# Kernel optimization log

Measured on AMD Instinct MI355X. Metric: run time of the kernel, lower is better.

The kernel has to match this reference:

```python
import jax, jax.numpy as jnp
import numpy as np

N_NODES = 100000
N_EDGES = 1600000


def spmm(edge_index, edge_vals, x, n_nodes):
    # adj @ x with adj in COO form: out[dst] += val * x[src]
    src = edge_index[0]
    dst = edge_index[1]
    gathered = x[src] * edge_vals[:, None]  # [E, F]
    return jax.ops.segment_sum(gathered, dst, num_segments=n_nodes)


def setup_inputs() -> dict:
    key = jax.random.key(0)
    ks = jax.random.split(key, 8)
    x = jax.random.normal(ks[0], (N_NODES, 512), dtype=jnp.float32)
    edge_index = jax.random.randint(ks[1], (2, N_EDGES), 0, N_NODES, dtype=jnp.int64)
    edge_vals = jax.random.uniform(ks[2], (N_EDGES,), dtype=jnp.float32)
    # xavier-uniform style weights, zero biases (as in initialize_weights)
    def xavier(k, fan_in, fan_out):
        lim = float(np.sqrt(6.0 / (fan_in + fan_out)))
        return jax.random.uniform(k, (fan_in, fan_out), minval=-lim, maxval=lim, dtype=jnp.float32)
    W1 = xavier(ks[3], 512, 128)
    b1 = jnp.zeros((128,), jnp.float32)
    W2 = xavier(ks[4], 128, 64)
    b2 = jnp.zeros((64,), jnp.float32)
    W3 = xavier(ks[5], 64, 16)
    b3 = jnp.zeros((16,), jnp.float32)
    return {"x": x, "edge_index": edge_index, "edge_vals": edge_vals,
            "W1": W1, "b1": b1, "W2": W2, "b2": b2, "W3": W3, "b3": b3}


def reference(x, edge_index, edge_vals, W1, b1, W2, b2, W3, b3):
    n = x.shape[0]
    h = jax.nn.relu(spmm(edge_index, edge_vals, x @ W1 + b1, n))
    h = jax.nn.relu(spmm(edge_index, edge_vals, h @ W2 + b2, n))
    logits = spmm(edge_index, edge_vals, h @ W3 + b3, n)
    logp = jax.nn.log_softmax(logits, axis=1)
    return jnp.argmax(logp, axis=1)
```

## Files before the change

### kernel.cpp

```cpp
#include <hip/hip_runtime.h>

typedef _Float16 half8 __attribute__((ext_vector_type(8)));
typedef float floatx4 __attribute__((ext_vector_type(4)));

#define BSHIFT 7
#define BMASK 127
#define EPB 8192
#define P2CAP 4096

__device__ __forceinline__ void g2lds16(const void* g, void* l) {
    __builtin_amdgcn_global_load_lds(
        (const __attribute__((address_space(1))) void*)(unsigned long long)g,
        (__attribute__((address_space(3))) void*)(unsigned int)(unsigned long long)l,
        16, 0, 0);
}

__global__ __launch_bounds__(256) void k1_prep_hist(const float* __restrict__ W1,
                                                    const float* __restrict__ W2,
                                                    _Float16* __restrict__ w1hi,
                                                    _Float16* __restrict__ w1lo,
                                                    _Float16* __restrict__ w2hi,
                                                    _Float16* __restrict__ w2lo,
                                                    const int* __restrict__ dst,
                                                    int* __restrict__ hist,
                                                    int E, int NBUCK) {
    __shared__ int lh[1024];
    int b = blockIdx.x, t = threadIdx.x;
    if (b < 256) {
        int tid = b * 256 + t;
        int n = tid >> 9;
        int k = tid & 511;
        float w = W1[(size_t)k * 128 + n];
        _Float16 h = (_Float16)w;
        w1hi[tid] = h;
        w1lo[tid] = (_Float16)(w - (float)h);
        return;
    }
    if (b < 288) {
        int tid = (b - 256) * 256 + t;
        int n = tid >> 7;
        int k = tid & 127;
        float w = W2[(size_t)k * 64 + n];
        _Float16 h = (_Float16)w;
        w2hi[tid] = h;
        w2lo[tid] = (_Float16)(w - (float)h);
        return;
    }
    int bb = b - 288;
    for (int k = t; k < NBUCK; k += 256) lh[k] = 0;
    __syncthreads();
    int e0 = bb * EPB;
    int eend = min(e0 + EPB, E);
    for (int i = e0 + t; i < eend; i += 256)
        atomicAdd(&lh[dst[i] >> BSHIFT], 1);
    __syncthreads();
    for (int k = t; k < NBUCK; k += 256) hist[(size_t)bb * NBUCK + k] = lh[k];
}

__global__ __launch_bounds__(256) void k2_scanA(const int* __restrict__ hist,
                                                int* __restrict__ blockOff,
                                                int* __restrict__ btot,
                                                int NBLK, int NBUCK) {
    __shared__ int s[256];
    int k = blockIdx.x;
    int t = threadIdx.x;
    int carry = 0;
    for (int base = 0; base < NBLK; base += 256) {
        int b = base + t;
        int c = (b < NBLK) ? hist[(size_t)b * NBUCK + k] : 0;
        s[t] = c;
        __syncthreads();
        for (int off = 1; off < 256; off <<= 1) {
            int v = (t >= off) ? s[t - off] : 0;
            __syncthreads();
            s[t] += v;
            __syncthreads();
        }
        if (b < NBLK) blockOff[(size_t)b * NBUCK + k] = carry + s[t] - c;
        carry += s[255];
        __syncthreads();
    }
    if (t == 0) btot[k] = carry;
}

__global__ __launch_bounds__(1024) void k2b_bscan(const int* __restrict__ btot,
                                                  int* __restrict__ bstart,
                                                  int* __restrict__ rowptr,
                                                  int NBUCK, int M, int E) {
    __shared__ int s[1024];
    int tid = threadIdx.x;
    int v = (tid < NBUCK) ? btot[tid] : 0;
    s[tid] = v;
    __syncthreads();
    for (int off = 1; off < 1024; off <<= 1) {
        int t = (tid >= off) ? s[tid - off] : 0;
        __syncthreads();
        s[tid] += t;
        __syncthreads();
    }
    if (tid < NBUCK) bstart[tid] = s[tid] - v;
    if (tid == 0) rowptr[M] = E;
}


__device__ __forceinline__ void p1d_body(int b, const int* __restrict__ src,
                                         const int* __restrict__ dst,
                                         const float* __restrict__ val,
                                         const int* __restrict__ bstart,
                                         const int* __restrict__ blockOff,
                                         int2* __restrict__ tmp,
                                         int E, int NBUCK, int* cur) {
    int t = threadIdx.x;
    for (int k = t; k < NBUCK; k += 256)
        cur[k] = bstart[k] + blockOff[(size_t)b * NBUCK + k];
    __syncthreads();
    int e0 = b * EPB;
    int eend = min(e0 + EPB, E);
    for (int i = e0 + t; i < eend; i += 256) {
        int d = dst[i];
        int p = atomicAdd(&cur[d >> BSHIFT], 1);
        int2 pk;
        pk.x = src[i] | ((d & BMASK) << 20);
        pk.y = __float_as_int(val[i]);
        tmp[p] = pk;
    }
}

__device__ __forceinline__ void p2_body(int k, const int2* __restrict__ tmp,
                                        const int* __restrict__ bstart,
                                        const int* __restrict__ btot,
                                        int* __restrict__ rowptr,
                                        int2* __restrict__ ssv, int M, char* lds) {
    int2* ebuf = (int2*)lds;
    int* h    = (int*)(lds + 32768);
    int* sc   = (int*)(lds + 33280);
    int* curs = (int*)(lds + 33792);
    int t = threadIdx.x;
    int base = bstart[k], n = btot[k];
    for (int j = t; j < 128; j += 256) h[j] = 0;
    __syncthreads();
    int nl = min(n, P2CAP);
    for (int i = t; i < nl; i += 256) {
        int2 e = tmp[base + i];
        ebuf[i] = e;
        atomicAdd(&h[e.x >> 20], 1);
    }
    for (int i = P2CAP + t; i < n; i += 256) {
        int2 e = tmp[base + i];
        atomicAdd(&h[e.x >> 20], 1);
    }
    __syncthreads();
    if (t < 128) sc[t] = h[t];
    __syncthreads();
    for (int off = 1; off < 128; off <<= 1) {
        int v = (t < 128 && t >= off) ? sc[t - off] : 0;
        __syncthreads();
        if (t < 128) sc[t] += v;
        __syncthreads();
    }
    if (t < 128) {
        int node = (k << BSHIFT) + t;
        int excl = sc[t] - h[t];
        if (node < M) rowptr[node] = base + excl;
        curs[t] = excl;
    }
    __syncthreads();
    for (int i = t; i < nl; i += 256) {
        int2 e = ebuf[i];
        int p = atomicAdd(&curs[e.x >> 20], 1);
        int2 o; o.x = e.x & 0xFFFFF; o.y = e.y;
        ssv[base + p] = o;
    }
    for (int i = P2CAP + t; i < n; i += 256) {
        int2 e = tmp[base + i];
        int p = atomicAdd(&curs[e.x >> 20], 1);
        int2 o; o.x = e.x & 0xFFFFF; o.y = e.y;
        ssv[base + p] = o;
    }
}


__device__ __forceinline__ void split8(float4 f0, float4 f1, half8& h, half8& l) {
    float f[8] = {f0.x, f0.y, f0.z, f0.w, f1.x, f1.y, f1.z, f1.w};
#pragma unroll
    for (int j = 0; j < 8; ++j) {
        _Float16 hi = (_Float16)f[j];
        h[j] = hi;
        l[j] = (_Float16)(f[j] - (float)hi);
    }
}


__device__ __forceinline__ void gemm1_body(int bm, char* smem,
                                           const float* __restrict__ X,
                                           const _Float16* __restrict__ Whi,
                                           const _Float16* __restrict__ Wlo,
                                           const float* __restrict__ bias,
                                           float* __restrict__ out, int M) {
    int t = threadIdx.x;
    int w = t >> 6;
    int lane = t & 63;
    int quad = lane >> 4;
    int l16 = lane & 15;
    int m0 = bm + w * 32;

    int ra0 = min(m0 + l16, M - 1);
    int ra1 = min(m0 + 16 + l16, M - 1);
    const float* a0p = X + (size_t)ra0 * 512 + quad * 8;
    const float* a1p = X + (size_t)ra1 * 512 + quad * 8;

    int chunk0 = w * 4;
    const _Float16* gsrc[4];
#pragma unroll
    for (int c = 0; c < 4; ++c) {
        int idx = (chunk0 + c) * 1024 + lane * 16;
        int sec = idx >> 13;
        int row = (idx & 8191) >> 6;
        int kch = (idx >> 4) & 3;
        gsrc[c] = (sec ? Wlo : Whi) + (size_t)row * 512 + kch * 8;
    }
#pragma unroll
    for (int c = 0; c < 4; ++c)
        g2lds16(gsrc[c], smem + (chunk0 + c) * 1024);
    float4 af00 = *(const float4*)(a0p);
    float4 af01 = *(const float4*)(a0p + 4);
    float4 af10 = *(const float4*)(a1p);
    float4 af11 = *(const float4*)(a1p + 4);

    floatx4 acc[2][8];
#pragma unroll
    for (int mt = 0; mt < 2; ++mt)
#pragma unroll
        for (int nt = 0; nt < 8; ++nt) acc[mt][nt] = (floatx4){0.f, 0.f, 0.f, 0.f};

    for (int i = 0; i < 16; ++i) {
        int k0 = i * 32;
        __syncthreads();
        if (i < 15) {
            char* nbuf = smem + ((i + 1) & 1) * 16384;
#pragma unroll
            for (int c = 0; c < 4; ++c)
                g2lds16(gsrc[c] + k0 + 32, nbuf + (chunk0 + c) * 1024);
        }
        float4 nf00 = af00, nf01 = af01, nf10 = af10, nf11 = af11;
        if (i < 15) {
            nf00 = *(const float4*)(a0p + k0 + 32);
            nf01 = *(const float4*)(a0p + k0 + 36);
            nf10 = *(const float4*)(a1p + k0 + 32);
            nf11 = *(const float4*)(a1p + k0 + 36);
        }
        const char* buf = smem + (i & 1) * 16384;
        half8 bh[8], bl[8];
#pragma unroll
        for (int nt = 0; nt < 8; ++nt) {
            int off = (nt * 16 + l16) * 64 + quad * 16;
            bh[nt] = *(const half8*)(buf + off);
            bl[nt] = *(const half8*)(buf + 8192 + off);
        }
        half8 ah0, al0, ah1, al1;
        split8(af00, af01, ah0, al0);
        split8(af10, af11, ah1, al1);
#pragma unroll
        for (int nt = 0; nt < 8; ++nt) {
            acc[0][nt] = __builtin_amdgcn_mfma_f32_16x16x32_f16(ah0, bh[nt], acc[0][nt], 0, 0, 0);
            acc[1][nt] = __builtin_amdgcn_mfma_f32_16x16x32_f16(ah1, bh[nt], acc[1][nt], 0, 0, 0);
            acc[0][nt] = __builtin_amdgcn_mfma_f32_16x16x32_f16(ah0, bl[nt], acc[0][nt], 0, 0, 0);
            acc[1][nt] = __builtin_amdgcn_mfma_f32_16x16x32_f16(ah1, bl[nt], acc[1][nt], 0, 0, 0);
            acc[0][nt] = __builtin_amdgcn_mfma_f32_16x16x32_f16(al0, bh[nt], acc[0][nt], 0, 0, 0);
            acc[1][nt] = __builtin_amdgcn_mfma_f32_16x16x32_f16(al1, bh[nt], acc[1][nt], 0, 0, 0);
        }
        af00 = nf00; af01 = nf01; af10 = nf10; af11 = nf11;
    }

#pragma unroll
    for (int nt = 0; nt < 8; ++nt) {
        int col = nt * 16 + l16;
        float bv = bias[col];
#pragma unroll
        for (int mt = 0; mt < 2; ++mt)
#pragma unroll
            for (int r = 0; r < 4; ++r) {
                int row = m0 + mt * 16 + quad * 4 + r;
                if (row < M) out[(size_t)row * 128 + col] = acc[mt][nt][r] + bv;
            }
    }
}

__global__ __launch_bounds__(256) void k3_p1d_gemm1a(const int* __restrict__ src,
                                                     const int* __restrict__ dst,
                                                     const float* __restrict__ val,
                                                     const int* __restrict__ bstart,
                                                     const int* __restrict__ blockOff,
                                                     int2* __restrict__ tmp,
                                                     int E, int NBUCK, int NBLK,
                                                     const float* __restrict__ X,
                                                     const _Float16* __restrict__ Whi,
                                                     const _Float16* __restrict__ Wlo,
                                                     const float* __restrict__ bias,
                                                     float* __restrict__ out, int M) {
    __shared__ __align__(16) char lds[32768];
    int b = blockIdx.x;
    if (b < NBLK) {
        p1d_body(b, src, dst, val, bstart, blockOff, tmp, E, NBUCK, (int*)lds);
        return;
    }
    gemm1_body((b - NBLK) * 128, lds, X, Whi, Wlo, bias, out, M);
}

__global__ __launch_bounds__(256) void k4_p2_gemm1b(const int2* __restrict__ tmp,
                                                    const int* __restrict__ bstart,
                                                    const int* __restrict__ btot,
                                                    int* __restrict__ rowptr,
                                                    int2* __restrict__ ssv,
                                                    int M, int NBUCK, int g1a,
                                                    const float* __restrict__ X,
                                                    const _Float16* __restrict__ Whi,
                                                    const _Float16* __restrict__ Wlo,
                                                    const float* __restrict__ bias,
                                                    float* __restrict__ out) {
    __shared__ __align__(16) char lds[34304];
    int b = blockIdx.x;
    if (b < NBUCK) {
        p2_body(b, tmp, bstart, btot, rowptr, ssv, M, lds);
        return;
    }
    gemm1_body((g1a + b - NBUCK) * 128, lds, X, Whi, Wlo, bias, out, M);
}


__global__ __launch_bounds__(256) void gemm2_mfma(const float* __restrict__ H,
                                                  const _Float16* __restrict__ Whi,
                                                  const _Float16* __restrict__ Wlo,
                                                  const float* __restrict__ bias,
                                                  float* __restrict__ out, int M) {
    __shared__ char smem[2 * 64 * 320];
    int t = threadIdx.x;
#pragma unroll
    for (int i = 0; i < 4; ++i) {
        int gidx = i * 256 + t;
        int row = gidx >> 4, col = gidx & 15;
        *(float4*)(smem + row * 320 + col * 16) = ((const float4*)Whi)[gidx];
        *(float4*)(smem + 20480 + row * 320 + col * 16) = ((const float4*)Wlo)[gidx];
    }
    __syncthreads();

    int w = t >> 6;
    int lane = t & 63;
    int quad = lane >> 4;
    int l16 = lane & 15;
    int m0 = blockIdx.x * 128 + w * 32;
    int ra0 = min(m0 + l16, M - 1);
    int ra1 = min(m0 + 16 + l16, M - 1);
    const float* a0p = H + (size_t)ra0 * 128 + quad * 8;
    const float* a1p = H + (size_t)ra1 * 128 + quad * 8;

    floatx4 acc[2][4];
#pragma unroll
    for (int mt = 0; mt < 2; ++mt)
#pragma unroll
        for (int nt = 0; nt < 4; ++nt) acc[mt][nt] = (floatx4){0.f, 0.f, 0.f, 0.f};

#pragma unroll
    for (int k0 = 0; k0 < 128; k0 += 32) {
        float4 af00 = *(const float4*)(a0p + k0);
        float4 af01 = *(const float4*)(a0p + k0 + 4);
        float4 af10 = *(const float4*)(a1p + k0);
        float4 af11 = *(const float4*)(a1p + k0 + 4);
        af00.x = fmaxf(af00.x, 0.f); af00.y = fmaxf(af00.y, 0.f);
        af00.z = fmaxf(af00.z, 0.f); af00.w = fmaxf(af00.w, 0.f);
        af01.x = fmaxf(af01.x, 0.f); af01.y = fmaxf(af01.y, 0.f);
        af01.z = fmaxf(af01.z, 0.f); af01.w = fmaxf(af01.w, 0.f);
        af10.x = fmaxf(af10.x, 0.f); af10.y = fmaxf(af10.y, 0.f);
        af10.z = fmaxf(af10.z, 0.f); af10.w = fmaxf(af10.w, 0.f);
        af11.x = fmaxf(af11.x, 0.f); af11.y = fmaxf(af11.y, 0.f);
        af11.z = fmaxf(af11.z, 0.f); af11.w = fmaxf(af11.w, 0.f);
        half8 bh[4], bl[4];
#pragma unroll
        for (int nt = 0; nt < 4; ++nt) {
            int off = (nt * 16 + l16) * 320 + k0 * 2 + quad * 16;
            bh[nt] = *(const half8*)(smem + off);
            bl[nt] = *(const half8*)(smem + 20480 + off);
        }
        half8 ah0, al0, ah1, al1;
        split8(af00, af01, ah0, al0);
        split8(af10, af11, ah1, al1);
#pragma unroll
        for (int nt = 0; nt < 4; ++nt) {
            acc[0][nt] = __builtin_amdgcn_mfma_f32_16x16x32_f16(ah0, bh[nt], acc[0][nt], 0, 0, 0);
            acc[1][nt] = __builtin_amdgcn_mfma_f32_16x16x32_f16(ah1, bh[nt], acc[1][nt], 0, 0, 0);
            acc[0][nt] = __builtin_amdgcn_mfma_f32_16x16x32_f16(ah0, bl[nt], acc[0][nt], 0, 0, 0);
            acc[1][nt] = __builtin_amdgcn_mfma_f32_16x16x32_f16(ah1, bl[nt], acc[1][nt], 0, 0, 0);
            acc[0][nt] = __builtin_amdgcn_mfma_f32_16x16x32_f16(al0, bh[nt], acc[0][nt], 0, 0, 0);
            acc[1][nt] = __builtin_amdgcn_mfma_f32_16x16x32_f16(al1, bh[nt], acc[1][nt], 0, 0, 0);
        }
    }

#pragma unroll
    for (int nt = 0; nt < 4; ++nt) {
        int col = nt * 16 + l16;
        float bv = bias[col];
#pragma unroll
        for (int mt = 0; mt < 2; ++mt)
#pragma unroll
            for (int r = 0; r < 4; ++r) {
                int row = m0 + mt * 16 + quad * 4 + r;
                if (row < M) out[(size_t)row * 64 + col] = acc[mt][nt][r] + bv;
            }
    }
}


__global__ __launch_bounds__(256) void gemm3(const float* __restrict__ H,
                                             const float* __restrict__ W,
                                             const float* __restrict__ bias,
                                             float* __restrict__ out, int M) {
    __shared__ float Ws[64 * 16];
    __shared__ float Xs[32 * 68];
    int t = threadIdx.x;
    int m0 = blockIdx.x * 32;
    ((float4*)Ws)[t] = ((const float4*)W)[t];
#pragma unroll
    for (int i = 0; i < 2; i++) {
        int idx = t + i * 256;
        int gi = idx * 4;
        int row = gi >> 6, col = gi & 63;
        float4 v = make_float4(0.f, 0.f, 0.f, 0.f);
        if (m0 + row < M) v = *(const float4*)(H + (size_t)(m0 + row) * 64 + col);
        v.x = fmaxf(v.x, 0.f); v.y = fmaxf(v.y, 0.f);
        v.z = fmaxf(v.z, 0.f); v.w = fmaxf(v.w, 0.f);
        *(float4*)&Xs[row * 68 + col] = v;
    }
    __syncthreads();
    int node = t >> 3;
    int j = t & 7;
    float a0 = 0.f, a1 = 0.f;
#pragma unroll 8
    for (int k = 0; k < 64; ++k) {
        float xv = Xs[node * 68 + k];
        a0 += xv * Ws[k * 16 + j * 2];
        a1 += xv * Ws[k * 16 + j * 2 + 1];
    }
    int row = m0 + node;
    if (row < M) {
        a0 += bias[j * 2];
        a1 += bias[j * 2 + 1];
        float2 r = make_float2(a0, a1);
        *(float2*)(out + (size_t)row * 16 + j * 2) = r;
    }
}


__global__ __launch_bounds__(256) void spmm128(const int* __restrict__ rowptr,
                                               const int2* __restrict__ ssv,
                                               const float* __restrict__ T,
                                               float* __restrict__ H, int N) {
    int lane = threadIdx.x & 63;
    int node = __builtin_amdgcn_readfirstlane(blockIdx.x * 4 + (threadIdx.x >> 6));
    if (node >= N) return;
    int beg = rowptr[node], end = rowptr[node + 1];
    int half = lane >> 5;
    int c4 = (lane & 31) << 2;
    float4 acc = make_float4(0.f, 0.f, 0.f, 0.f);
    int i = beg;
    int cnt = end - beg;
    int n8 = beg + (cnt & ~7);
    for (; i < n8; i += 8) {
#pragma unroll
        for (int u = 0; u < 4; ++u) {
            int2 e = ssv[i + 2 * u + half];
            float v = __int_as_float(e.y);
            float4 xv = *(const float4*)(T + ((size_t)e.x << 7) + c4);
            acc.x += v * xv.x; acc.y += v * xv.y;
            acc.z += v * xv.z; acc.w += v * xv.w;
        }
    }
    int n2 = beg + (cnt & ~1);
    for (; i < n2; i += 2) {
        int2 e = ssv[i + half];
        float v = __int_as_float(e.y);
        float4 xv = *(const float4*)(T + ((size_t)e.x << 7) + c4);
        acc.x += v * xv.x; acc.y += v * xv.y;
        acc.z += v * xv.z; acc.w += v * xv.w;
    }
    if (i < end) {
        int2 e = ssv[i];
        float v = half ? 0.f : __int_as_float(e.y);
        float4 xv = *(const float4*)(T + ((size_t)e.x << 7) + c4);
        acc.x += v * xv.x; acc.y += v * xv.y;
        acc.z += v * xv.z; acc.w += v * xv.w;
    }
    acc.x += __shfl_xor(acc.x, 32, 64);
    acc.y += __shfl_xor(acc.y, 32, 64);
    acc.z += __shfl_xor(acc.z, 32, 64);
    acc.w += __shfl_xor(acc.w, 32, 64);
    if (half == 0)
        *(float4*)(H + ((size_t)node << 7) + c4) = acc;
}

__global__ __launch_bounds__(256) void spmm64(const int* __restrict__ rowptr,
                                              const int2* __restrict__ ssv,
                                              const float* __restrict__ T,
                                              float* __restrict__ H, int N) {
    int lane = threadIdx.x & 63;
    int node = __builtin_amdgcn_readfirstlane(blockIdx.x * 4 + (threadIdx.x >> 6));
    if (node >= N) return;
    int beg = rowptr[node], end = rowptr[node + 1];
    int es = lane >> 4;
    int c4 = (lane & 15) << 2;
    float4 acc = make_float4(0.f, 0.f, 0.f, 0.f);
    int i = beg;
    int cnt = end - beg;
    int n8 = beg + (cnt & ~7);
    for (; i < n8; i += 8) {
#pragma unroll
        for (int u = 0; u < 2; ++u) {
            int2 e = ssv[i + 4 * u + es];
            float v = __int_as_float(e.y);
            float4 xv = *(const float4*)(T + ((size_t)e.x << 6) + c4);
            acc.x += v * xv.x; acc.y += v * xv.y;
            acc.z += v * xv.z; acc.w += v * xv.w;
        }
    }
    int n4 = beg + (cnt & ~3);
    for (; i < n4; i += 4) {
        int2 e = ssv[i + es];
        float v = __int_as_float(e.y);
        float4 xv = *(const float4*)(T + ((size_t)e.x << 6) + c4);
        acc.x += v * xv.x; acc.y += v * xv.y;
        acc.z += v * xv.z; acc.w += v * xv.w;
    }
    if (i < end) {
        int idx = i + es;
        int2 e = ssv[idx < end ? idx : i];
        float v = (idx < end) ? __int_as_float(e.y) : 0.f;
        float4 xv = *(const float4*)(T + ((size_t)e.x << 6) + c4);
        acc.x += v * xv.x; acc.y += v * xv.y;
        acc.z += v * xv.z; acc.w += v * xv.w;
    }
    acc.x += __shfl_xor(acc.x, 16, 64);
    acc.y += __shfl_xor(acc.y, 16, 64);
    acc.z += __shfl_xor(acc.z, 16, 64);
    acc.w += __shfl_xor(acc.w, 16, 64);
    acc.x += __shfl_xor(acc.x, 32, 64);
    acc.y += __shfl_xor(acc.y, 32, 64);
    acc.z += __shfl_xor(acc.z, 32, 64);
    acc.w += __shfl_xor(acc.w, 32, 64);
    if (lane < 16)
        *(float4*)(H + ((size_t)node << 6) + c4) = acc;
}

__global__ __launch_bounds__(256) void spmm_argmax(const int* __restrict__ rowptr,
                                                   const int2* __restrict__ ssv,
                                                   const float* __restrict__ T,
                                                   int* __restrict__ out, int N) {
    int t = threadIdx.x;
    int node = blockIdx.x * 64 + (t >> 2);
    int q = t & 3;
    int c4 = q << 2;
    int beg = 0, end = 0;
    if (node < N) { beg = rowptr[node]; end = rowptr[node + 1]; }
    float4 acc = make_float4(0.f, 0.f, 0.f, 0.f);
    int i = beg;
    int cnt = end - beg;
    int n4 = beg + (cnt & ~3);
    for (; i < n4; i += 4) {
#pragma unroll
        for (int u = 0; u < 4; ++u) {
            int2 e = ssv[i + u];
            float v = __int_as_float(e.y);
            float4 xv = *(const float4*)(T + ((size_t)e.x << 4) + c4);
            acc.x += v * xv.x; acc.y += v * xv.y;
            acc.z += v * xv.z; acc.w += v * xv.w;
        }
    }
    for (; i < end; ++i) {
        int2 e = ssv[i];
        float v = __int_as_float(e.y);
        float4 xv = *(const float4*)(T + ((size_t)e.x << 4) + c4);
        acc.x += v * xv.x; acc.y += v * xv.y;
        acc.z += v * xv.z; acc.w += v * xv.w;
    }
    float bv = acc.x; int bi = c4;
    if (acc.y > bv) { bv = acc.y; bi = c4 + 1; }
    if (acc.z > bv) { bv = acc.z; bi = c4 + 2; }
    if (acc.w > bv) { bv = acc.w; bi = c4 + 3; }
#pragma unroll
    for (int off = 1; off <= 2; off <<= 1) {
        float ov = __shfl_xor(bv, off, 64);
        int oi = __shfl_xor(bi, off, 64);
        if (ov > bv || (ov == bv && oi < bi)) { bv = ov; bi = oi; }
    }
    if (node < N && q == 0) out[node] = bi;
}


extern "C" void kernel_launch(void* const* d_in, const int* in_sizes, int n_in,
                              void* d_out, int out_size, void* d_ws, size_t ws_size,
                              hipStream_t stream) {
    const float* x  = (const float*)d_in[0];
    const int*   ei = (const int*)d_in[1];
    const float* ev = (const float*)d_in[2];
    const float* W1 = (const float*)d_in[3];
    const float* b1 = (const float*)d_in[4];
    const float* W2 = (const float*)d_in[5];
    const float* b2 = (const float*)d_in[6];
    const float* W3 = (const float*)d_in[7];
    const float* b3 = (const float*)d_in[8];
    int* out = (int*)d_out;

    int M = in_sizes[0] / 512;
    int E = in_sizes[2];
    const int* src = ei;
    const int* dst = ei + E;

    int NBUCK = (M + BMASK) >> BSHIFT;
    int NBLK  = (E + EPB - 1) / EPB;

    char* ws = (char*)d_ws;
    size_t off = 0;
    auto alloc = [&](size_t bytes) {
        size_t o = off;
        off += (bytes + 255) & ~(size_t)255;
        return o;
    };
    float*    tA      = (float*)(ws + alloc((size_t)M * 128 * 4));
    float*    hB      = (float*)(ws + alloc((size_t)M * 128 * 4));
    int2*     ssv     = (int2*) (ws + alloc((size_t)E * 8));
    int*      rowptr  = (int*)  (ws + alloc((size_t)(M + 1) * 4));
    int*      hist    = (int*)  (ws + alloc((size_t)NBLK * NBUCK * 4));
    int*      blockOff= (int*)  (ws + alloc((size_t)NBLK * NBUCK * 4));
    int*      btot    = (int*)  (ws + alloc((size_t)NBUCK * 4));
    int*      bstart  = (int*)  (ws + alloc((size_t)NBUCK * 4));
    _Float16* w1hi    = (_Float16*)(ws + alloc(512 * 128 * 2));
    _Float16* w1lo    = (_Float16*)(ws + alloc(512 * 128 * 2));
    _Float16* w2hi    = (_Float16*)(ws + alloc(128 * 64 * 2));
    _Float16* w2lo    = (_Float16*)(ws + alloc(128 * 64 * 2));
    int2*     tmp     = (int2*)hB;

    int G1  = (M + 127) / 128;
    int G1a = G1 / 2;
    int G1b = G1 - G1a;

    k1_prep_hist<<<288 + NBLK, 256, 0, stream>>>(W1, W2, w1hi, w1lo, w2hi, w2lo,
                                                 dst, hist, E, NBUCK);
    k2_scanA<<<NBUCK, 256, 0, stream>>>(hist, blockOff, btot, NBLK, NBUCK);
    k2b_bscan<<<1, 1024, 0, stream>>>(btot, bstart, rowptr, NBUCK, M, E);
    k3_p1d_gemm1a<<<NBLK + G1a, 256, 0, stream>>>(src, dst, ev, bstart, blockOff, tmp,
                                                  E, NBUCK, NBLK,
                                                  x, w1hi, w1lo, b1, tA, M);
    k4_p2_gemm1b<<<NBUCK + G1b, 256, 0, stream>>>(tmp, bstart, btot, rowptr, ssv,
                                                  M, NBUCK, G1a,
                                                  x, w1hi, w1lo, b1, tA);

    spmm128<<<(M + 3) / 4, 256, 0, stream>>>(rowptr, ssv, tA, hB, M);
    gemm2_mfma<<<(M + 127) / 128, 256, 0, stream>>>(hB, w2hi, w2lo, b2, tA, M);
    spmm64<<<(M + 3) / 4, 256, 0, stream>>>(rowptr, ssv, tA, hB, M);
    gemm3<<<(M + 31) / 32, 256, 0, stream>>>(hB, W3, b3, tA, M);
    spmm_argmax<<<(M + 63) / 64, 256, 0, stream>>>(rowptr, ssv, tA, out, M);
}
```

Baseline: 644.6 us.

## Fuse SpMM aggregation with following GEMM via LDS-staged rows

Merges spmm128 with gemm2 and spmm64 with gemm3 into two kernels. Each block aggregates neighbour rows for a 64- or 32-node tile, applies ReLU and stores the result in LDS, then runs the dense projection directly from LDS. This removes the intermediate hidden-activation round-trips through global memory and two kernel launches. In exchange, each wave now processes nodes serially inside the block, there are fewer blocks, and the GEMM2 weights are read from global memory rather than staged in LDS, so latency hiding for the irregular gathers may suffer.

```diff
diff --git a/kernel.cpp b/kernel.cpp
--- a/kernel.cpp
+++ b/kernel.cpp
@@ -328,226 +328,208 @@
 }
 
 
-__global__ __launch_bounds__(256) void gemm2_mfma(const float* __restrict__ H,
-                                                  const _Float16* __restrict__ Whi,
-                                                  const _Float16* __restrict__ Wlo,
-                                                  const float* __restrict__ bias,
-                                                  float* __restrict__ out, int M) {
-    __shared__ char smem[2 * 64 * 320];
+__global__ __launch_bounds__(256) void k5_spmm128_gemm2(const int* __restrict__ rowptr,
+                                                        const int2* __restrict__ ssv,
+                                                        const float* __restrict__ T,
+                                                        const _Float16* __restrict__ Whi,
+                                                        const _Float16* __restrict__ Wlo,
+                                                        const float* __restrict__ bias,
+                                                        float* __restrict__ out, int M) {
+    __shared__ float Xs[64][132];
     int t = threadIdx.x;
-#pragma unroll
-    for (int i = 0; i < 4; ++i) {
-        int gidx = i * 256 + t;
-        int row = gidx >> 4, col = gidx & 15;
-        *(float4*)(smem + row * 320 + col * 16) = ((const float4*)Whi)[gidx];
-        *(float4*)(smem + 20480 + row * 320 + col * 16) = ((const float4*)Wlo)[gidx];
-    }
-    __syncthreads();
-
-    int w = t >> 6;
+    int wv = t >> 6;
     int lane = t & 63;
+    int nbase = blockIdx.x * 64;
+    int half = lane >> 5;
+    int c4 = (lane & 31) << 2;
+
+    for (int j = 0; j < 16; ++j) {
+        int local = wv * 16 + j;
+        int node = nbase + local;
+        float4 acc = make_float4(0.f, 0.f, 0.f, 0.f);
+        if (node < M) {
+            int beg = rowptr[node], end = rowptr[node + 1];
+            int i = beg;
+            int cnt = end - beg;
+            int n8 = beg + (cnt & ~7);
+            for (; i < n8; i += 8) {
+#pragma unroll
+                for (int u = 0; u < 4; ++u) {
+                    int2 e = ssv[i + 2 * u + half];
+                    float v = __int_as_float(e.y);
+                    float4 xv = *(const float4*)(T + ((size_t)e.x << 7) + c4);
+                    acc.x += v * xv.x; acc.y += v * xv.y;
+                    acc.z += v * xv.z; acc.w += v * xv.w;
+                }
+            }
+            int n2 = beg + (cnt & ~1);
+            for (; i < n2; i += 2) {
+                int2 e = ssv[i + half];
+                float v = __int_as_float(e.y);
+                float4 xv = *(const float4*)(T + ((size_t)e.x << 7) + c4);
+                acc.x += v * xv.x; acc.y += v * xv.y;
+                acc.z += v * xv.z; acc.w += v * xv.w;
+            }
+            if (i < end) {
+                int2 e = ssv[i];
+                float v = half ? 0.f : __int_as_float(e.y);
+                float4 xv = *(const float4*)(T + ((size_t)e.x << 7) + c4);
+                acc.x += v * xv.x; acc.y += v * xv.y;
+                acc.z += v * xv.z; acc.w += v * xv.w;
+            }
+        }
+        acc.x += __shfl_xor(acc.x, 32, 64);
+        acc.y += __shfl_xor(acc.y, 32, 64);
+        acc.z += __shfl_xor(acc.z, 32, 64);
+        acc.w += __shfl_xor(acc.w, 32, 64);
+        if (half == 0) {
+            Xs[local][c4 + 0] = fmaxf(acc.x, 0.f);
+            Xs[local][c4 + 1] = fmaxf(acc.y, 0.f);
+            Xs[local][c4 + 2] = fmaxf(acc.z, 0.f);
+            Xs[local][c4 + 3] = fmaxf(acc.w, 0.f);
+        }
+    }
+    __syncthreads();
+
     int quad = lane >> 4;
     int l16 = lane & 15;
-    int m0 = blockIdx.x * 128 + w * 32;
-    int ra0 = min(m0 + l16, M - 1);
-    int ra1 = min(m0 + 16 + l16, M - 1);
-    const float* a0p = H + (size_t)ra0 * 128 + quad * 8;
-    const float* a1p = H + (size_t)ra1 * 128 + quad * 8;
-
-    floatx4 acc[2][4];
+    int mr = (wv & 1) * 32;
+    int nc = (wv >> 1) * 32;
+    floatx4 acc2[2][2];
 #pragma unroll
     for (int mt = 0; mt < 2; ++mt)
 #pragma unroll
-        for (int nt = 0; nt < 4; ++nt) acc[mt][nt] = (floatx4){0.f, 0.f, 0.f, 0.f};
+        for (int nt = 0; nt < 2; ++nt) acc2[mt][nt] = (floatx4){0.f, 0.f, 0.f, 0.f};
 
 #pragma unroll
     for (int k0 = 0; k0 < 128; k0 += 32) {
-        float4 af00 = *(const float4*)(a0p + k0);
-        float4 af01 = *(const float4*)(a0p + k0 + 4);
-        float4 af10 = *(const float4*)(a1p + k0);
-        float4 af11 = *(const float4*)(a1p + k0 + 4);
-        af00.x = fmaxf(af00.x, 0.f); af00.y = fmaxf(af00.y, 0.f);
-        af00.z = fmaxf(af00.z, 0.f); af00.w = fmaxf(af00.w, 0.f);
-        af01.x = fmaxf(af01.x, 0.f); af01.y = fmaxf(af01.y, 0.f);
-        af01.z = fmaxf(af01.z, 0.f); af01.w = fmaxf(af01.w, 0.f);
-        af10.x = fmaxf(af10.x, 0.f); af10.y = fmaxf(af10.y, 0.f);
-        af10.z = fmaxf(af10.z, 0.f); af10.w = fmaxf(af10.w, 0.f);
-        af11.x = fmaxf(af11.x, 0.f); af11.y = fmaxf(af11.y, 0.f);
-        af11.z = fmaxf(af11.z, 0.f); af11.w = fmaxf(af11.w, 0.f);
-        half8 bh[4], bl[4];
-#pragma unroll
-        for (int nt = 0; nt < 4; ++nt) {
-            int off = (nt * 16 + l16) * 320 + k0 * 2 + quad * 16;
-            bh[nt] = *(const half8*)(smem + off);
-            bl[nt] = *(const half8*)(smem + 20480 + off);
+        float4 af00 = *(const float4*)&Xs[mr + l16][k0 + quad * 8];
+        float4 af01 = *(const float4*)&Xs[mr + l16][k0 + quad * 8 + 4];
+        float4 af10 = *(const float4*)&Xs[mr + 16 + l16][k0 + quad * 8];
+        float4 af11 = *(const float4*)&Xs[mr + 16 + l16][k0 + quad * 8 + 4];
+        half8 bh[2], bl[2];
+#pragma unroll
+        for (int nt = 0; nt < 2; ++nt) {
+            int n = nc + nt * 16 + l16;
+            bh[nt] = *(const half8*)(Whi + (size_t)n * 128 + k0 + quad * 8);
+            bl[nt] = *(const half8*)(Wlo + (size_t)n * 128 + k0 + quad * 8);
         }
         half8 ah0, al0, ah1, al1;
         split8(af00, af01, ah0, al0);
         split8(af10, af11, ah1, al1);
 #pragma unroll
-        for (int nt = 0; nt < 4; ++nt) {
-            acc[0][nt] = __builtin_amdgcn_mfma_f32_16x16x32_f16(ah0, bh[nt], acc[0][nt], 0, 0, 0);
-            acc[1][nt] = __builtin_amdgcn_mfma_f32_16x16x32_f16(ah1, bh[nt], acc[1][nt], 0, 0, 0);
-            acc[0][nt] = __builtin_amdgcn_mfma_f32_16x16x32_f16(ah0, bl[nt], acc[0][nt], 0, 0, 0);
-            acc[1][nt] = __builtin_amdgcn_mfma_f32_16x16x32_f16(ah1, bl[nt], acc[1][nt], 0, 0, 0);
-            acc[0][nt] = __builtin_amdgcn_mfma_f32_16x16x32_f16(al0, bh[nt], acc[0][nt], 0, 0, 0);
-            acc[1][nt] = __builtin_amdgcn_mfma_f32_16x16x32_f16(al1, bh[nt], acc[1][nt], 0, 0, 0);
-        }
-    }
-
-#pragma unroll
-    for (int nt = 0; nt < 4; ++nt) {
-        int col = nt * 16 + l16;
+        for (int nt = 0; nt < 2; ++nt) {
+            acc2[0][nt] = __builtin_amdgcn_mfma_f32_16x16x32_f16(ah0, bh[nt], acc2[0][nt], 0, 0, 0);
+            acc2[1][nt] = __builtin_amdgcn_mfma_f32_16x16x32_f16(ah1, bh[nt], acc2[1][nt], 0, 0, 0);
+            acc2[0][nt] = __builtin_amdgcn_mfma_f32_16x16x32_f16(ah0, bl[nt], acc2[0][nt], 0, 0, 0);
+            acc2[1][nt] = __builtin_amdgcn_mfma_f32_16x16x32_f16(ah1, bl[nt], acc2[1][nt], 0, 0, 0);
+            acc2[0][nt] = __builtin_amdgcn_mfma_f32_16x16x32_f16(al0, bh[nt], acc2[0][nt], 0, 0, 0);
+            acc2[1][nt] = __builtin_amdgcn_mfma_f32_16x16x32_f16(al1, bh[nt], acc2[1][nt], 0, 0, 0);
+        }
+    }
+
+#pragma unroll
+    for (int nt = 0; nt < 2; ++nt) {
+        int col = nc + nt * 16 + l16;
         float bv = bias[col];
 #pragma unroll
         for (int mt = 0; mt < 2; ++mt)
 #pragma unroll
             for (int r = 0; r < 4; ++r) {
-                int row = m0 + mt * 16 + quad * 4 + r;
-                if (row < M) out[(size_t)row * 64 + col] = acc[mt][nt][r] + bv;
-            }
-    }
-}
-
-
-__global__ __launch_bounds__(256) void gemm3(const float* __restrict__ H,
-                                             const float* __restrict__ W,
-                                             const float* __restrict__ bias,
-                                             float* __restrict__ out, int M) {
+                int row = nbase + mr + mt * 16 + quad * 4 + r;
+                if (row < M) out[(size_t)row * 64 + col] = acc2[mt][nt][r] + bv;
+            }
+    }
+}
+
+
+__global__ __launch_bounds__(256) void k6_spmm64_gemm3(const int* __restrict__ rowptr,
+                                                       const int2* __restrict__ ssv,
+                                                       const float* __restrict__ T,
+                                                       const float* __restrict__ W,
+                                                       const float* __restrict__ bias,
+                                                       float* __restrict__ out, int M) {
     __shared__ float Ws[64 * 16];
     __shared__ float Xs[32 * 68];
     int t = threadIdx.x;
-    int m0 = blockIdx.x * 32;
     ((float4*)Ws)[t] = ((const float4*)W)[t];
-#pragma unroll
-    for (int i = 0; i < 2; i++) {
-        int idx = t + i * 256;
-        int gi = idx * 4;
-        int row = gi >> 6, col = gi & 63;
-        float4 v = make_float4(0.f, 0.f, 0.f, 0.f);
-        if (m0 + row < M) v = *(const float4*)(H + (size_t)(m0 + row) * 64 + col);
-        v.x = fmaxf(v.x, 0.f); v.y = fmaxf(v.y, 0.f);
-        v.z = fmaxf(v.z, 0.f); v.w = fmaxf(v.w, 0.f);
-        *(float4*)&Xs[row * 68 + col] = v;
-    }
-    __syncthreads();
-    int node = t >> 3;
-    int j = t & 7;
+    int wv = t >> 6;
+    int lane = t & 63;
+    int nbase = blockIdx.x * 32;
+    int es = lane >> 4;
+    int c4 = (lane & 15) << 2;
+
+    for (int j = 0; j < 8; ++j) {
+        int local = wv * 8 + j;
+        int node = nbase + local;
+        float4 acc = make_float4(0.f, 0.f, 0.f, 0.f);
+        if (node < M) {
+            int beg = rowptr[node], end = rowptr[node + 1];
+            int i = beg;
+            int cnt = end - beg;
+            int n8 = beg + (cnt & ~7);
+            for (; i < n8; i += 8) {
+#pragma unroll
+                for (int u = 0; u < 2; ++u) {
+                    int2 e = ssv[i + 4 * u + es];
+                    float v = __int_as_float(e.y);
+                    float4 xv = *(const float4*)(T + ((size_t)e.x << 6) + c4);
+                    acc.x += v * xv.x; acc.y += v * xv.y;
+                    acc.z += v * xv.z; acc.w += v * xv.w;
+                }
+            }
+            int n4 = beg + (cnt & ~3);
+            for (; i < n4; i += 4) {
+                int2 e = ssv[i + es];
+                float v = __int_as_float(e.y);
+                float4 xv = *(const float4*)(T + ((size_t)e.x << 6) + c4);
+                acc.x += v * xv.x; acc.y += v * xv.y;
+                acc.z += v * xv.z; acc.w += v * xv.w;
+            }
+            if (i < end) {
+                int idx = i + es;
+                int2 e = ssv[idx < end ? idx : i];
+                float v = (idx < end) ? __int_as_float(e.y) : 0.f;
+                float4 xv = *(const float4*)(T + ((size_t)e.x << 6) + c4);
+                acc.x += v * xv.x; acc.y += v * xv.y;
+                acc.z += v * xv.z; acc.w += v * xv.w;
+            }
+        }
+        acc.x += __shfl_xor(acc.x, 16, 64);
+        acc.y += __shfl_xor(acc.y, 16, 64);
+        acc.z += __shfl_xor(acc.z, 16, 64);
+        acc.w += __shfl_xor(acc.w, 16, 64);
+        acc.x += __shfl_xor(acc.x, 32, 64);
+        acc.y += __shfl_xor(acc.y, 32, 64);
+        acc.z += __shfl_xor(acc.z, 32, 64);
+        acc.w += __shfl_xor(acc.w, 32, 64);
+        if (lane < 16) {
+            Xs[local * 68 + c4 + 0] = fmaxf(acc.x, 0.f);
+            Xs[local * 68 + c4 + 1] = fmaxf(acc.y, 0.f);
+            Xs[local * 68 + c4 + 2] = fmaxf(acc.z, 0.f);
+            Xs[local * 68 + c4 + 3] = fmaxf(acc.w, 0.f);
+        }
+    }
+    __syncthreads();
+
+    int node2 = t >> 3;
+    int jj = t & 7;
     float a0 = 0.f, a1 = 0.f;
 #pragma unroll 8
     for (int k = 0; k < 64; ++k) {
-        float xv = Xs[node * 68 + k];
-        a0 += xv * Ws[k * 16 + j * 2];
-        a1 += xv * Ws[k * 16 + j * 2 + 1];
-    }
-    int row = m0 + node;
+        float xv = Xs[node2 * 68 + k];
+        a0 += xv * Ws[k * 16 + jj * 2];
+        a1 += xv * Ws[k * 16 + jj * 2 + 1];
+    }
+    int row = nbase + node2;
     if (row < M) {
-        a0 += bias[j * 2];
-        a1 += bias[j * 2 + 1];
+        a0 += bias[jj * 2];
+        a1 += bias[jj * 2 + 1];
         float2 r = make_float2(a0, a1);
-        *(float2*)(out + (size_t)row * 16 + j * 2) = r;
-    }
-}
-
-
-__global__ __launch_bounds__(256) void spmm128(const int* __restrict__ rowptr,
-                                               const int2* __restrict__ ssv,
-                                               const float* __restrict__ T,
-                                               float* __restrict__ H, int N) {
-    int lane = threadIdx.x & 63;
-    int node = __builtin_amdgcn_readfirstlane(blockIdx.x * 4 + (threadIdx.x >> 6));
-    if (node >= N) return;
-    int beg = rowptr[node], end = rowptr[node + 1];
-    int half = lane >> 5;
-    int c4 = (lane & 31) << 2;
-    float4 acc = make_float4(0.f, 0.f, 0.f, 0.f);
-    int i = beg;
-    int cnt = end - beg;
-    int n8 = beg + (cnt & ~7);
-    for (; i < n8; i += 8) {
-#pragma unroll
-        for (int u = 0; u < 4; ++u) {
-            int2 e = ssv[i + 2 * u + half];
-            float v = __int_as_float(e.y);
-            float4 xv = *(const float4*)(T + ((size_t)e.x << 7) + c4);
-            acc.x += v * xv.x; acc.y += v * xv.y;
-            acc.z += v * xv.z; acc.w += v * xv.w;
-        }
-    }
-    int n2 = beg + (cnt & ~1);
-    for (; i < n2; i += 2) {
-        int2 e = ssv[i + half];
-        float v = __int_as_float(e.y);
-        float4 xv = *(const float4*)(T + ((size_t)e.x << 7) + c4);
-        acc.x += v * xv.x; acc.y += v * xv.y;
-        acc.z += v * xv.z; acc.w += v * xv.w;
-    }
-    if (i < end) {
-        int2 e = ssv[i];
-        float v = half ? 0.f : __int_as_float(e.y);
-        float4 xv = *(const float4*)(T + ((size_t)e.x << 7) + c4);
-        acc.x += v * xv.x; acc.y += v * xv.y;
-        acc.z += v * xv.z; acc.w += v * xv.w;
-    }
-    acc.x += __shfl_xor(acc.x, 32, 64);
-    acc.y += __shfl_xor(acc.y, 32, 64);
-    acc.z += __shfl_xor(acc.z, 32, 64);
-    acc.w += __shfl_xor(acc.w, 32, 64);
-    if (half == 0)
-        *(float4*)(H + ((size_t)node << 7) + c4) = acc;
-}
-
-__global__ __launch_bounds__(256) void spmm64(const int* __restrict__ rowptr,
-                                              const int2* __restrict__ ssv,
-                                              const float* __restrict__ T,
-                                              float* __restrict__ H, int N) {
-    int lane = threadIdx.x & 63;
-    int node = __builtin_amdgcn_readfirstlane(blockIdx.x * 4 + (threadIdx.x >> 6));
-    if (node >= N) return;
-    int beg = rowptr[node], end = rowptr[node + 1];
-    int es = lane >> 4;
-    int c4 = (lane & 15) << 2;
-    float4 acc = make_float4(0.f, 0.f, 0.f, 0.f);
-    int i = beg;
-    int cnt = end - beg;
-    int n8 = beg + (cnt & ~7);
-    for (; i < n8; i += 8) {
-#pragma unroll
-        for (int u = 0; u < 2; ++u) {
-            int2 e = ssv[i + 4 * u + es];
-            float v = __int_as_float(e.y);
-            float4 xv = *(const float4*)(T + ((size_t)e.x << 6) + c4);
-            acc.x += v * xv.x; acc.y += v * xv.y;
-            acc.z += v * xv.z; acc.w += v * xv.w;
-        }
-    }
-    int n4 = beg + (cnt & ~3);
-    for (; i < n4; i += 4) {
-        int2 e = ssv[i + es];
-        float v = __int_as_float(e.y);
-        float4 xv = *(const float4*)(T + ((size_t)e.x << 6) + c4);
-        acc.x += v * xv.x; acc.y += v * xv.y;
-        acc.z += v * xv.z; acc.w += v * xv.w;
-    }
-    if (i < end) {
-        int idx = i + es;
-        int2 e = ssv[idx < end ? idx : i];
-        float v = (idx < end) ? __int_as_float(e.y) : 0.f;
-        float4 xv = *(const float4*)(T + ((size_t)e.x << 6) + c4);
-        acc.x += v * xv.x; acc.y += v * xv.y;
-        acc.z += v * xv.z; acc.w += v * xv.w;
-    }
-    acc.x += __shfl_xor(acc.x, 16, 64);
-    acc.y += __shfl_xor(acc.y, 16, 64);
-    acc.z += __shfl_xor(acc.z, 16, 64);
-    acc.w += __shfl_xor(acc.w, 16, 64);
-    acc.x += __shfl_xor(acc.x, 32, 64);
-    acc.y += __shfl_xor(acc.y, 32, 64);
-    acc.z += __shfl_xor(acc.z, 32, 64);
-    acc.w += __shfl_xor(acc.w, 32, 64);
-    if (lane < 16)
-        *(float4*)(H + ((size_t)node << 6) + c4) = acc;
-}
+        *(float2*)(out + (size_t)row * 16 + jj * 2) = r;
+    }
+}
+
 
 __global__ __launch_bounds__(256) void spmm_argmax(const int* __restrict__ rowptr,
                                                    const int2* __restrict__ ssv,
@@ -652,9 +634,10 @@
                                                   M, NBUCK, G1a,
                                                   x, w1hi, w1lo, b1, tA);
 
-    spmm128<<<(M + 3) / 4, 256, 0, stream>>>(rowptr, ssv, tA, hB, M);
-    gemm2_mfma<<<(M + 127) / 128, 256, 0, stream>>>(hB, w2hi, w2lo, b2, tA, M);
-    spmm64<<<(M + 3) / 4, 256, 0, stream>>>(rowptr, ssv, tA, hB, M);
-    gemm3<<<(M + 31) / 32, 256, 0, stream>>>(hB, W3, b3, tA, M);
+    k5_spmm128_gemm2<<<(M + 63) / 64, 256, 0, stream>>>(rowptr, ssv, tA,
+                                                        w2hi, w2lo, b2,
+                                                        hB, M);
+    k6_spmm64_gemm3<<<(M + 31) / 32, 256, 0, stream>>>(rowptr, ssv, hB,
+                                                       W3, b3, tA, M);
     spmm_argmax<<<(M + 63) / 64, 256, 0, stream>>>(rowptr, ssv, tA, out, M);
 }
```

Result: no change. 645.3 us (+0.1%).
